# Performance work log

Hardware: AMD Instinct MI355X
Metric: run time of the kernel (lower is better)

## Reference

```python
import jax, jax.numpy as jnp
import numpy as np

B, T, C = 8, 2048, 1024
H, K = 16, 31  # num_heads, kernel_size; head_size = C // H = 64


def setup_inputs() -> dict:
    key = jax.random.key(0)
    ks = jax.random.split(key, 3)
    x = jax.random.normal(ks[0], (B, T, C), dtype=jnp.float32)
    Wk = jax.random.normal(ks[1], (C, 2 * C), dtype=jnp.float32) * 0.02
    bk = jnp.zeros((2 * C,), dtype=jnp.float32)
    Wck = jax.random.normal(ks[2], (C, K * H), dtype=jnp.float32) * 0.02
    bck = jnp.zeros((K * H,), dtype=jnp.float32)
    gamma = jnp.ones((C,), dtype=jnp.float32)
    beta = jnp.zeros((C,), dtype=jnp.float32)
    conv_bias = jnp.zeros((C,), dtype=jnp.float32)
    return {"x": x, "Wk": Wk, "bk": bk, "Wck": Wck, "bck": bck,
            "gamma": gamma, "beta": beta, "conv_bias": conv_bias}


def _layernorm(x, g, b, eps=1e-5):
    mu = jnp.mean(x, axis=-1, keepdims=True)
    var = jnp.mean(jnp.square(x - mu), axis=-1, keepdims=True)
    return (x - mu) * jax.lax.rsqrt(var + eps) * g + b


def reference(x, Wk, bk, Wck, bck, gamma, beta, conv_bias):
    b, t, c = x.shape
    hd = c // H  # head size
    h = _layernorm(x, gamma, beta)
    pre = h @ Wk + bk                      # [B,T,2C]
    a, gte = jnp.split(pre, 2, axis=-1)
    k = a * jax.nn.sigmoid(gte)            # GLU -> [B,T,C]
    w = (k @ Wck + bck).reshape(b, t, H, K)
    w = jax.nn.softmax(w, axis=-1)         # per-token per-head kernel
    pad = K // 2
    kp = jnp.pad(k, ((0, 0), (pad, pad), (0, 0))).reshape(b, t + 2 * pad, H, hd)
    # depthwise dynamic conv: sum over K shifted slices (no im2col blowup)
    out = sum(w[:, :, :, i:i + 1] * kp[:, i:i + t] for i in range(K))  # [B,T,H,hd]
    out = out.reshape(b, t, c) + conv_bias + x  # bias + residual
    return out
```

## Files before the change

kernel.cpp:

```cpp
#include <hip/hip_runtime.h>


typedef __bf16 bf16_t;
typedef __attribute__((ext_vector_type(8))) __bf16 bf16x8;
typedef __attribute__((ext_vector_type(4))) __bf16 bf16x4;
typedef __attribute__((ext_vector_type(4))) float f32x4;

__device__ __forceinline__ void gload_lds16(const void* g, void* l) {
  void* gg = const_cast<void*>(g);
  __builtin_amdgcn_global_load_lds(
      (__attribute__((address_space(1))) unsigned int*)gg,
      (__attribute__((address_space(3))) unsigned int*)l, 16, 0, 0);
}

__global__ __launch_bounds__(256) void prep_wk(const float* __restrict__ Wk,
                                               bf16_t* __restrict__ WT) {
  int c = blockIdx.x;
  int s = (c & 1) ? 1024 + (c >> 1) : (c >> 1);
  int k = threadIdx.x * 4;
  bf16x4 v;
#pragma unroll
  for (int j = 0; j < 4; ++j) v[j] = (bf16_t)Wk[(size_t)(k + j) * 2048 + s];
  *(bf16x4*)&WT[(size_t)c * 1024 + k] = v;
}

__global__ __launch_bounds__(256) void prep_wck(const float* __restrict__ Wck,
                                                bf16_t* __restrict__ WT) {
  int n = blockIdx.x;
  int k = threadIdx.x * 4;
  bf16x4 v;
#pragma unroll
  for (int j = 0; j < 4; ++j)
    v[j] = (n < 496) ? (bf16_t)Wck[(size_t)(k + j) * 496 + n] : (bf16_t)(0.f);
  *(bf16x4*)&WT[(size_t)n * 1024 + k] = v;
}

__global__ __launch_bounds__(256) void ln_kernel(const float* __restrict__ x,
                                                 const float* __restrict__ gamma,
                                                 const float* __restrict__ beta,
                                                 bf16_t* __restrict__ h) {
  int row = blockIdx.x;
  int tid = threadIdx.x;
  int lane = tid & 63, wid = tid >> 6;
  const float4* xr = (const float4*)(x + (size_t)row * 1024);
  float4 v = xr[tid];
  __shared__ float red[4];
  __shared__ float bc[2];
  float s = v.x + v.y + v.z + v.w;
#pragma unroll
  for (int off = 32; off > 0; off >>= 1) s += __shfl_down(s, off);
  if (lane == 0) red[wid] = s;
  __syncthreads();
  if (tid == 0) bc[0] = (red[0] + red[1] + red[2] + red[3]) * (1.f / 1024.f);
  __syncthreads();
  float mu = bc[0];
  float dx = v.x - mu, dy = v.y - mu, dz = v.z - mu, dw = v.w - mu;
  float s2 = dx * dx + dy * dy + dz * dz + dw * dw;
#pragma unroll
  for (int off = 32; off > 0; off >>= 1) s2 += __shfl_down(s2, off);
  if (lane == 0) red[wid] = s2;
  __syncthreads();
  if (tid == 0)
    bc[1] = rsqrtf((red[0] + red[1] + red[2] + red[3]) * (1.f / 1024.f) + 1e-5f);
  __syncthreads();
  float rs = bc[1];
  const float4* g4 = (const float4*)gamma;
  const float4* b4 = (const float4*)beta;
  float4 gv = g4[tid], bv = b4[tid];
  bf16x4 o;
  o[0] = (bf16_t)(dx * rs * gv.x + bv.x);
  o[1] = (bf16_t)(dy * rs * gv.y + bv.y);
  o[2] = (bf16_t)(dz * rs * gv.z + bv.z);
  o[3] = (bf16_t)(dw * rs * gv.w + bv.w);
  *(bf16x4*)&h[(size_t)row * 1024 + tid * 4] = o;
}

template <int EPI>
__global__ __launch_bounds__(256, 2) void gemm128(const bf16_t* __restrict__ Ag,
                                                  const bf16_t* __restrict__ Bg,
                                                  const float* __restrict__ bias,
                                                  void* __restrict__ outp) {
  __shared__ bf16_t As[2][128 * 32];
  __shared__ bf16_t Bs[2][128 * 32];
  int tid = threadIdx.x;
  int lane = tid & 63;
  int wid = tid >> 6;
  int wr = wid >> 1, wc = wid & 1;
  int n0 = blockIdx.x * 128;
  int m0 = blockIdx.y * 128;

  f32x4 acc[4][4] = {};

#define STAGE(bufi, kt)                                                         \
  {                                                                             \
    _Pragma("unroll") for (int s_ = 0; s_ < 2; ++s_) {                          \
      int idx = (tid + s_ * 256) * 8;                                           \
      int row = idx >> 5;                                                       \
      int col = idx & 31;                                                       \
      gload_lds16(Ag + (size_t)(m0 + row) * 1024 + (kt) + col, &As[bufi][idx]); \
      gload_lds16(Bg + (size_t)(n0 + row) * 1024 + (kt) + col, &Bs[bufi][idx]); \
    }                                                                           \
  }

#define COMPUTE(bufi)                                                           \
  {                                                                             \
    int ko = (lane >> 4) * 8;                                                   \
    int rl = lane & 15;                                                         \
    bf16x8 af[4], bb[4];                                                        \
    _Pragma("unroll") for (int m_ = 0; m_ < 4; ++m_)                            \
        af[m_] = *(const bf16x8*)&As[bufi][(wr * 64 + m_ * 16 + rl) * 32 + ko]; \
    _Pragma("unroll") for (int n_ = 0; n_ < 4; ++n_)                            \
        bb[n_] = *(const bf16x8*)&Bs[bufi][(wc * 64 + n_ * 16 + rl) * 32 + ko]; \
    _Pragma("unroll") for (int m_ = 0; m_ < 4; ++m_)                            \
        _Pragma("unroll") for (int n_ = 0; n_ < 4; ++n_)                        \
            acc[m_][n_] = __builtin_amdgcn_mfma_f32_16x16x32_bf16(              \
                af[m_], bb[n_], acc[m_][n_], 0, 0, 0);                          \
  }

  STAGE(0, 0);
  __syncthreads();
  int buf = 0;
  for (int kt = 32; kt < 1024; kt += 32) {
    STAGE(buf ^ 1, kt);
    COMPUTE(buf);
    __syncthreads();
    buf ^= 1;
  }
  COMPUTE(buf);

#pragma unroll
  for (int m_ = 0; m_ < 4; ++m_) {
    int row = m0 + wr * 64 + m_ * 16 + ((lane >> 4) << 2);
#pragma unroll
    for (int n_ = 0; n_ < 4; ++n_) {
      int col = n0 + wc * 64 + n_ * 16 + (lane & 15);
      if constexpr (EPI == 0) {
        int src = (col & 1) ? 1024 + (col >> 1) : (col >> 1);
        float bv = bias[src];
#pragma unroll
        for (int j = 0; j < 4; ++j) {
          float v = acc[m_][n_][j] + bv;
          float g = __shfl_xor(v, 1);
          if (!(col & 1)) {
            float kv = v / (1.f + __expf(-g));
            ((bf16_t*)outp)[(size_t)(row + j) * 1024 + (col >> 1)] = (bf16_t)kv;
          }
        }
      } else {
        float bv = (col < 496) ? bias[col] : 0.f;
#pragma unroll
        for (int j = 0; j < 4; ++j)
          ((float*)outp)[(size_t)(row + j) * 512 + col] = acc[m_][n_][j] + bv;
      }
    }
  }
#undef STAGE
#undef COMPUTE
}

__global__ __launch_bounds__(256) void conv_kernel(const bf16_t* __restrict__ Kin,
                                                   const float* __restrict__ logits,
                                                   const float* __restrict__ x,
                                                   const float* __restrict__ conv_bias,
                                                   float* __restrict__ out) {
  __shared__ bf16_t ks[94][64];
  __shared__ float wls[64][32];
  int tid = threadIdx.x;
  int t0 = blockIdx.x * 64;
  int hh = blockIdx.y;
  int b = blockIdx.z;

  for (int i = tid; i < 94 * 8; i += 256) {
    int r = i >> 3;
    int seg = (i & 7) * 8;
    int t = t0 - 15 + r;
    bf16x8 v = {};
    if (t >= 0 && t < 2048)
      v = *(const bf16x8*)&Kin[((size_t)b * 2048 + t) * 1024 + hh * 64 + seg];
    *(bf16x8*)&ks[r][seg] = v;
  }
  if (tid < 64) {
    int t = t0 + tid;
    const float* lp = logits + ((size_t)b * 2048 + t) * 512 + hh * 31;
    float l[31];
    float mx = -1e30f;
#pragma unroll
    for (int i = 0; i < 31; ++i) { l[i] = lp[i]; mx = fmaxf(mx, l[i]); }
    float ssum = 0.f;
#pragma unroll
    for (int i = 0; i < 31; ++i) { l[i] = __expf(l[i] - mx); ssum += l[i]; }
    float inv = 1.f / ssum;
#pragma unroll
    for (int i = 0; i < 31; ++i) wls[tid][i] = l[i] * inv;
  }
  __syncthreads();

  int lane = tid & 63;
  int tq = tid >> 6;
  float win[46];
#pragma unroll
  for (int j = 0; j < 46; ++j) win[j] = (float)ks[tq * 16 + j][lane];
  float cb = conv_bias[hh * 64 + lane];
#pragma unroll
  for (int j = 0; j < 16; ++j) {
    int trow = tq * 16 + j;
    float wv[31];
#pragma unroll
    for (int i4 = 0; i4 < 7; ++i4) {
      f32x4 w4 = *(const f32x4*)&wls[trow][i4 * 4];
      wv[i4 * 4 + 0] = w4[0]; wv[i4 * 4 + 1] = w4[1];
      wv[i4 * 4 + 2] = w4[2]; wv[i4 * 4 + 3] = w4[3];
    }
    wv[28] = wls[trow][28]; wv[29] = wls[trow][29]; wv[30] = wls[trow][30];
    float a = 0.f;
#pragma unroll
    for (int i = 0; i < 31; ++i) a += wv[i] * win[j + i];
    size_t off = ((size_t)b * 2048 + t0 + trow) * 1024 + hh * 64 + lane;
    out[off] = a + cb + x[off];
  }
}

extern "C" void kernel_launch(void* const* d_in, const int* in_sizes, int n_in,
                              void* d_out, int out_size, void* d_ws, size_t ws_size,
                              hipStream_t stream) {
  const float* x         = (const float*)d_in[0];
  const float* Wk        = (const float*)d_in[1];
  const float* bk        = (const float*)d_in[2];
  const float* Wck       = (const float*)d_in[3];
  const float* bck       = (const float*)d_in[4];
  const float* gamma     = (const float*)d_in[5];
  const float* beta      = (const float*)d_in[6];
  const float* conv_bias = (const float*)d_in[7];
  float* out = (float*)d_out;

  char* ws = (char*)d_ws;
  bf16_t* h      = (bf16_t*)(ws);
  bf16_t* kbuf   = (bf16_t*)(ws + (33554432));
  bf16_t* WT1    = (bf16_t*)(ws + (67108864));
  bf16_t* WT2    = (bf16_t*)(ws + (71303168));
  float*  logits = (float*)(ws + (72351744));

  prep_wk<<<2048, 256, 0, stream>>>(Wk, WT1);
  prep_wck<<<512, 256, 0, stream>>>(Wck, WT2);
  ln_kernel<<<16384, 256, 0, stream>>>(x, gamma, beta, h);
  gemm128<0><<<dim3(16, 128), 256, 0, stream>>>(h, WT1, bk, kbuf);
  gemm128<1><<<dim3(4, 128), 256, 0, stream>>>(kbuf, WT2, bck, logits);
  conv_kernel<<<dim3(32, 16, 8), 256, 0, stream>>>(kbuf, logits, x, conv_bias, out);
}
```

Measured before the change: 303.8 us.

## Replace GLU GEMM with 256x256-tile pipelined MFMA kernel using swizzled LDS

The large LayerNorm-output × Wk GEMM with fused GLU epilogue moves to a new kernel. It uses 256x256 output tiles, 512 threads, a K-step of 64 and the 16x16x32 bf16 MFMA. LDS is XOR-swizzled to avoid bank conflicts, and global-to-LDS loads are staged in phases interleaved with MFMA work, using explicit vmcnt waits and s_setprio. A block-index swizzle improves L2 locality. The aim is higher arithmetic intensity and better overlap of memory with compute. The cost is 128 KB of dynamic LDS per block, which limits occupancy, and much more intricate hand-scheduled synchronization.

```diff
diff --git a/kernel.cpp b/kernel.cpp
--- a/kernel.cpp
+++ b/kernel.cpp
@@ -75,11 +75,133 @@
   *(bf16x4*)&h[(size_t)row * 1024 + tid * 4] = o;
 }
 
-template <int EPI>
-__global__ __launch_bounds__(256, 2) void gemm128(const bf16_t* __restrict__ Ag,
-                                                  const bf16_t* __restrict__ Bg,
-                                                  const float* __restrict__ bias,
-                                                  void* __restrict__ outp) {
+__global__ __launch_bounds__(512, 2) void gemm256_glu(const bf16_t* __restrict__ Ag,
+                                                      const bf16_t* __restrict__ Bg,
+                                                      const float* __restrict__ bias,
+                                                      bf16_t* __restrict__ outp) {
+  extern __shared__ char smem[];
+  const int tid = threadIdx.x;
+  const int lane = tid & 63;
+  const int wid = tid >> 6;
+  const int wr = wid >> 2;
+  const int wc = wid & 3;
+
+  int bid = blockIdx.x;
+  int swz = (bid & 7) * 64 + (bid >> 3);
+  int m0 = (swz >> 3) * 256;
+  int n0 = (swz & 7) * 256;
+
+  const int xr = (lane & 7) << 4;
+  const int cs0 = (((lane >> 4) << 4) ^ xr);
+  const int cs1 = cs0 ^ 64;
+  const int aBase = wr * 16384 + (lane & 15) * 128;
+  const int bBase = 65536 + (wc >> 1) * 16384 + (wc & 1) * 8192 + (lane & 15) * 128;
+
+  const int sidx0 = tid, sidx1 = tid + 512;
+  const int srow0 = sidx0 >> 3, srow1 = sidx1 >> 3;
+  const int scol0 = ((((sidx0 & 7) << 4) ^ ((srow0 & 7) << 4)) >> 1);
+  const int scol1 = ((((sidx1 & 7) << 4) ^ ((srow1 & 7) << 4)) >> 1);
+  const int d0 = sidx0 * 16, d1 = sidx1 * 16;
+
+  f32x4 acc[8][4] = {};
+  bf16x8 bq[4][2];
+
+#define STAGE_A(buf, h_, kt)                                                          \
+  {                                                                                   \
+    gload_lds16(Ag + (size_t)(m0 + (h_)*128 + srow0) * 1024 + (kt) + scol0,           \
+                smem + (buf)*32768 + (h_)*16384 + d0);                                \
+    gload_lds16(Ag + (size_t)(m0 + (h_)*128 + srow1) * 1024 + (kt) + scol1,           \
+                smem + (buf)*32768 + (h_)*16384 + d1);                                \
+  }
+#define STAGE_B(buf, h_, kt)                                                          \
+  {                                                                                   \
+    gload_lds16(Bg + (size_t)(n0 + (h_)*128 + srow0) * 1024 + (kt) + scol0,           \
+                smem + 65536 + (buf)*32768 + (h_)*16384 + d0);                        \
+    gload_lds16(Bg + (size_t)(n0 + (h_)*128 + srow1) * 1024 + (kt) + scol1,           \
+                smem + 65536 + (buf)*32768 + (h_)*16384 + d1);                        \
+  }
+#define LDA(buf, f, s) (*(const bf16x8*)(smem + (buf)*32768 + aBase + (f)*2048 + ((s) ? cs1 : cs0)))
+#define LDB(buf, g, s) (*(const bf16x8*)(smem + bBase + (buf)*32768 + (g)*2048 + ((s) ? cs1 : cs0)))
+#define MFMA_(a, b, c) __builtin_amdgcn_mfma_f32_16x16x32_bf16(a, b, c, 0, 0, 0)
+
+#define PHASE(buf, f0, P0, STAGE_STMT, TAIL_VM)                                       \
+  {                                                                                   \
+    bf16x8 a00 = LDA(buf, f0, 0), a01 = LDA(buf, f0, 1);                              \
+    bf16x8 a10 = LDA(buf, (f0) + 1, 0), a11 = LDA(buf, (f0) + 1, 1);                  \
+    if (P0) {                                                                         \
+      _Pragma("unroll") for (int g = 0; g < 4; ++g) {                                 \
+        bq[g][0] = LDB(buf, g, 0);                                                    \
+        bq[g][1] = LDB(buf, g, 1);                                                    \
+      }                                                                               \
+    }                                                                                 \
+    STAGE_STMT;                                                                       \
+    __builtin_amdgcn_s_barrier();                                                     \
+    __builtin_amdgcn_s_setprio(1);                                                    \
+    _Pragma("unroll") for (int g = 0; g < 4; ++g) {                                   \
+      acc[f0][g] = MFMA_(a00, bq[g][0], acc[f0][g]);                                  \
+      acc[f0][g] = MFMA_(a01, bq[g][1], acc[f0][g]);                                  \
+      acc[(f0) + 1][g] = MFMA_(a10, bq[g][0], acc[(f0) + 1][g]);                      \
+      acc[(f0) + 1][g] = MFMA_(a11, bq[g][1], acc[(f0) + 1][g]);                      \
+    }                                                                                 \
+    __builtin_amdgcn_s_setprio(0);                                                    \
+    TAIL_VM;                                                                          \
+    __builtin_amdgcn_s_barrier();                                                     \
+  }
+
+  STAGE_B(0, 0, 0); STAGE_B(0, 1, 0); STAGE_A(0, 0, 0); STAGE_A(0, 1, 0);
+  STAGE_B(1, 0, 64); STAGE_B(1, 1, 64);
+  asm volatile("s_waitcnt vmcnt(4)" ::: "memory");
+  __builtin_amdgcn_s_barrier();
+
+  for (int t = 0; t < 14; ++t) {
+    const int buf = t & 1, nbuf = buf ^ 1;
+    const int ktA = (t + 1) * 64, ktB = (t + 2) * 64;
+    PHASE(buf, 0, 1, STAGE_A(nbuf, 0, ktA), ((void)0));
+    PHASE(buf, 2, 0, STAGE_A(nbuf, 1, ktA), ((void)0));
+    PHASE(buf, 4, 0, STAGE_B(buf, 0, ktB), ((void)0));
+    PHASE(buf, 6, 0, STAGE_B(buf, 1, ktB),
+          asm volatile("s_waitcnt vmcnt(4)" ::: "memory"));
+  }
+  PHASE(0, 0, 1, STAGE_A(1, 0, 960), ((void)0));
+  PHASE(0, 2, 0, STAGE_A(1, 1, 960), ((void)0));
+  PHASE(0, 4, 0, ((void)0), ((void)0));
+  PHASE(0, 6, 0, ((void)0), asm volatile("s_waitcnt vmcnt(0)" ::: "memory"));
+  PHASE(1, 0, 1, ((void)0), ((void)0));
+  PHASE(1, 2, 0, ((void)0), ((void)0));
+  PHASE(1, 4, 0, ((void)0), ((void)0));
+  PHASE(1, 6, 0, ((void)0), ((void)0));
+
+#pragma unroll
+  for (int f = 0; f < 8; ++f) {
+    int row = m0 + wr * 128 + f * 16 + ((lane >> 4) << 2);
+#pragma unroll
+    for (int g = 0; g < 4; ++g) {
+      int col = n0 + wc * 64 + g * 16 + (lane & 15);
+      int src = (col & 1) ? 1024 + (col >> 1) : (col >> 1);
+      float bv = bias[src];
+#pragma unroll
+      for (int j = 0; j < 4; ++j) {
+        float v = acc[f][g][j] + bv;
+        float gt = __shfl_xor(v, 1);
+        if (!(col & 1)) {
+          float kv = v / (1.f + __expf(-gt));
+          outp[(size_t)(row + j) * 1024 + (col >> 1)] = (bf16_t)kv;
+        }
+      }
+    }
+  }
+#undef STAGE_A
+#undef STAGE_B
+#undef LDA
+#undef LDB
+#undef MFMA_
+#undef PHASE
+}
+
+__global__ __launch_bounds__(256, 2) void gemm128_bias(const bf16_t* __restrict__ Ag,
+                                                       const bf16_t* __restrict__ Bg,
+                                                       const float* __restrict__ bias,
+                                                       float* __restrict__ outp) {
   __shared__ bf16_t As[2][128 * 32];
   __shared__ bf16_t Bs[2][128 * 32];
   int tid = threadIdx.x;
@@ -134,24 +256,10 @@
 #pragma unroll
     for (int n_ = 0; n_ < 4; ++n_) {
       int col = n0 + wc * 64 + n_ * 16 + (lane & 15);
-      if constexpr (EPI == 0) {
-        int src = (col & 1) ? 1024 + (col >> 1) : (col >> 1);
-        float bv = bias[src];
-#pragma unroll
-        for (int j = 0; j < 4; ++j) {
-          float v = acc[m_][n_][j] + bv;
-          float g = __shfl_xor(v, 1);
-          if (!(col & 1)) {
-            float kv = v / (1.f + __expf(-g));
-            ((bf16_t*)outp)[(size_t)(row + j) * 1024 + (col >> 1)] = (bf16_t)kv;
-          }
-        }
-      } else {
-        float bv = (col < 496) ? bias[col] : 0.f;
-#pragma unroll
-        for (int j = 0; j < 4; ++j)
-          ((float*)outp)[(size_t)(row + j) * 512 + col] = acc[m_][n_][j] + bv;
-      }
+      float bv = (col < 496) ? bias[col] : 0.f;
+#pragma unroll
+      for (int j = 0; j < 4; ++j)
+        outp[(size_t)(row + j) * 512 + col] = acc[m_][n_][j] + bv;
     }
   }
 #undef STAGE
@@ -240,10 +348,13 @@
   bf16_t* WT2    = (bf16_t*)(ws + (71303168));
   float*  logits = (float*)(ws + (72351744));
 
+  hipFuncSetAttribute((const void*)gemm256_glu,
+                      hipFuncAttributeMaxDynamicSharedMemorySize, 131072);
+
   prep_wk<<<2048, 256, 0, stream>>>(Wk, WT1);
   prep_wck<<<512, 256, 0, stream>>>(Wck, WT2);
   ln_kernel<<<16384, 256, 0, stream>>>(x, gamma, beta, h);
-  gemm128<0><<<dim3(16, 128), 256, 0, stream>>>(h, WT1, bk, kbuf);
-  gemm128<1><<<dim3(4, 128), 256, 0, stream>>>(kbuf, WT2, bck, logits);
+  gemm256_glu<<<512, 512, 131072, stream>>>(h, WT1, bk, kbuf);
+  gemm128_bias<<<dim3(4, 128), 256, 0, stream>>>(kbuf, WT2, bck, logits);
   conv_kernel<<<dim3(32, 16, 8), 256, 0, stream>>>(kbuf, logits, x, conv_bias, out);
 }
```

Result: faster. 292.7 us (-3.7%).
